# Kernel optimization log

Measured on AMD Instinct MI355X. Metric: run time of the kernel, lower is better.

The kernel has to match this reference:

```python
import jax, jax.numpy as jnp
import numpy as np

N = 50000      # nodes
E = 800000     # edges (before self loops)
IN = 128       # input_dim
H1, C1 = 4, 64   # conv1 heads, per-head channels (concat -> 256)
H2, C2 = 1, 64   # conv2 heads, per-head channels (concat=False -> 64)
EPS_BN = 1e-5
NEG_SLOPE = 0.2


def setup_inputs() -> dict:
    key = jax.random.key(0)
    ks = jax.random.split(key, 20)
    s = 0.05
    d = {}
    d["x"] = jax.random.normal(ks[0], (N, IN), dtype=jnp.float32)
    d["edge_index"] = jax.random.randint(ks[1], (2, E), 0, N, dtype=jnp.int32)
    # GATConv 1: lin weight [IN, H1*C1], att vectors [H1, C1], bias [H1*C1]
    d["W1"] = jax.random.normal(ks[2], (IN, H1 * C1), dtype=jnp.float32) * s
    d["a1_src"] = jax.random.normal(ks[3], (H1, C1), dtype=jnp.float32) * s
    d["a1_dst"] = jax.random.normal(ks[4], (H1, C1), dtype=jnp.float32) * s
    d["b1"] = jnp.zeros((H1 * C1,), jnp.float32)
    # GATConv 2 (concat=False): lin weight [H1*C1, H2*C2]
    d["W2"] = jax.random.normal(ks[5], (H1 * C1, H2 * C2), dtype=jnp.float32) * s
    d["a2_src"] = jax.random.normal(ks[6], (H2, C2), dtype=jnp.float32) * s
    d["a2_dst"] = jax.random.normal(ks[7], (H2, C2), dtype=jnp.float32) * s
    d["b2"] = jnp.zeros((C2,), jnp.float32)
    # projection Linear(output_dim -> input_dim)
    d["Wp"] = jax.random.normal(ks[8], (C2, IN), dtype=jnp.float32) * s
    d["bp"] = jnp.zeros((IN,), jnp.float32)
    # BatchNorm affine params
    d["g1"] = jnp.ones((H1 * C1,), jnp.float32); d["be1"] = jnp.zeros((H1 * C1,), jnp.float32)
    d["g2"] = jnp.ones((C2,), jnp.float32);      d["be2"] = jnp.zeros((C2,), jnp.float32)
    d["g3"] = jnp.ones((IN,), jnp.float32);      d["be3"] = jnp.zeros((IN,), jnp.float32)
    return d


def batch_norm(x, gamma, beta):
    mu = jnp.mean(x, axis=0, keepdims=True)
    var = jnp.var(x, axis=0, keepdims=True)
    return (x - mu) * jax.lax.rsqrt(var + EPS_BN) * gamma + beta


def gat_conv(x, src, dst, W, a_src, a_dst, bias, heads, out_ch, concat):
    n = x.shape[0]
    h = (x @ W).reshape(n, heads, out_ch)            # [N,H,C]
    alpha_s = jnp.einsum('nhc,hc->nh', h, a_src)     # [N,H]
    alpha_d = jnp.einsum('nhc,hc->nh', h, a_dst)
    e = jax.nn.leaky_relu(alpha_s[src] + alpha_d[dst], NEG_SLOPE)  # [E',H]
    # segment softmax over edges sharing the same destination node
    m = jax.ops.segment_max(e, dst, num_segments=n)
    m = jnp.where(jnp.isfinite(m), m, 0.0)
    ex = jnp.exp(e - m[dst])
    den = jax.ops.segment_sum(ex, dst, num_segments=n)
    alpha = ex / (den[dst] + 1e-16)                  # [E',H]
    msg = alpha[:, :, None] * h[src]                 # [E',H,C]
    out = jax.ops.segment_sum(msg, dst, num_segments=n)  # [N,H,C]
    if concat:
        out = out.reshape(n, heads * out_ch)
    else:
        out = out.mean(axis=1)
    return out + bias


def reference(x, edge_index, W1, a1_src, a1_dst, b1, W2, a2_src, a2_dst, b2,
              Wp, bp, g1, be1, g2, be2, g3, be3):
    n = x.shape[0]
    # PyG GATConv default add_self_loops=True
    loops = jnp.arange(n, dtype=edge_index.dtype)
    src = jnp.concatenate([edge_index[0], loops])
    dst = jnp.concatenate([edge_index[1], loops])
    h = gat_conv(x, src, dst, W1, a1_src, a1_dst, b1, H1, C1, True)
    h = jax.nn.elu(batch_norm(h, g1, be1))
    # dropout is a no-op in eval mode
    h = gat_conv(h, src, dst, W2, a2_src, a2_dst, b2, H2, C2, False)
    h = jax.nn.elu(batch_norm(h, g2, be2))
    h = h @ Wp + bp
    return batch_norm(h, g3, be3)
```

## Files before the change

kernel.cpp:

```cpp
#include <hip/hip_runtime.h>
#include <cstdint>
#include <cstddef>

#define NEG_SLOPE 0.2f
#define EPS_BN 1e-5f

typedef __bf16 bf16x8 __attribute__((ext_vector_type(8)));
typedef float  f32x4  __attribute__((ext_vector_type(4)));
typedef unsigned short ushort_t;

static __device__ __forceinline__ float lrelu(float x){ return x > 0.f ? x : NEG_SLOPE * x; }
static __device__ __forceinline__ float elu(float x){ return x > 0.f ? x : __expf(x) - 1.f; }

static __device__ __forceinline__ float bf2f(ushort_t u){
  union { unsigned i; float f; } c; c.i = ((unsigned)u) << 16; return c.f;
}
static __device__ __forceinline__ ushort_t f2bf(float f){
  unsigned u = __float_as_uint(f);
  u += 0x7fffu + ((u >> 16) & 1u);
  return (ushort_t)(u >> 16);
}
static __device__ __forceinline__ void unpk(unsigned u, float& lo, float& hi){
  lo = __uint_as_float(u << 16);
  hi = __uint_as_float(u & 0xffff0000u);
}

union BF8 { bf16x8 v; ushort_t u[8]; };

static inline int ceil_div(int a, int b){ return (a + b - 1) / b; }


__global__ void fill_u32_kernel(unsigned* __restrict__ p, unsigned v, int n){
  int i = blockIdx.x * 256 + threadIdx.x;
  if(i < n) p[i] = v;
}


__global__ void hist_kernel(const int* __restrict__ ei, int* __restrict__ deg, int E, int N){
  int e = blockIdx.x * 256 + threadIdx.x;
  if(e >= E + N) return;
  int d = (e < E) ? ei[E + e] : (e - E);
  atomicAdd(&deg[d], 1);
}

__global__ __launch_bounds__(256) void scan1_kernel(const int* __restrict__ deg, int* __restrict__ rowptr,
                                                    int* __restrict__ cur, int* __restrict__ partials,
                                                    unsigned* __restrict__ tick, int n){
  int t = threadIdx.x, lane = t & 63, wv = t >> 6;
  int base = blockIdx.x * 2048 + t * 8;
  int v[8]; int run = 0;
  #pragma unroll
  for(int k = 0; k < 8; k++){ int i = base + k; v[k] = (i < n) ? deg[i] : 0; run += v[k]; }
  int sc = run;
  #pragma unroll
  for(int off = 1; off < 64; off <<= 1){
    int u = __shfl_up(sc, off);
    if(lane >= off) sc += u;
  }
  __shared__ int wtot[4], woff[4];
  __shared__ bool slast;
  if(lane == 63) wtot[wv] = sc;
  __syncthreads();
  if(t == 0){
    int a = 0;
    #pragma unroll
    for(int i = 0; i < 4; i++){ woff[i] = a; a += wtot[i]; }
    partials[blockIdx.x] = a;
  }
  __syncthreads();
  int excl = (sc - run) + woff[wv];
  #pragma unroll
  for(int k = 0; k < 8; k++){
    int i = base + k;
    if(i < n){ cur[i] = excl; excl += v[k]; rowptr[i + 1] = excl; }
  }
  if(t == 0){
    __threadfence();
    slast = (atomicAdd(tick, 1u) == (unsigned)(gridDim.x - 1));
  }
  __syncthreads();
  if(slast && t < 64){
    int nb = gridDim.x;
    int pv = (t < nb) ? atomicAdd(&partials[t], 0) : 0;
    int psc = pv;
    #pragma unroll
    for(int off = 1; off < 64; off <<= 1){
      int u = __shfl_up(psc, off);
      if(t >= off) psc += u;
    }
    if(t < nb) partials[t] = psc - pv;
  }
}

__global__ void scan3_kernel(const int* __restrict__ partials, int* __restrict__ rowptr,
                             int* __restrict__ cur, int n){
  int i = blockIdx.x * 256 + threadIdx.x;
  if(i == 0) rowptr[0] = 0;
  if(i < n){
    int off = partials[i >> 11];
    rowptr[i + 1] += off;
    cur[i] += off;
  }
}

__global__ void scatter_kernel(const int* __restrict__ ei, int* __restrict__ cur,
                               int* __restrict__ col, int E, int N){
  int e = blockIdx.x * 256 + threadIdx.x;
  if(e >= E + N) return;
  int s, d;
  if(e < E){ s = ei[e]; d = ei[E + e]; } else { s = e - E; d = e - E; }
  int pos = atomicAdd(&cur[d], 1);
  col[pos] = s;
}


static __device__ void packW_body(const float* W, ushort_t* Wp, int K, int Nn, int idx){
  int lane = idx & 63;
  int rest = idx >> 6;
  int KS = K >> 5;
  int s = rest % KS, t = rest / KS;
  int n  = t * 16 + (lane & 15);
  int k0 = s * 32 + (lane >> 4) * 8;
  ushort_t tmp[8];
  #pragma unroll
  for(int j = 0; j < 8; j++) tmp[j] = f2bf(W[(size_t)(k0 + j) * Nn + n]);
  uint4 pk;
  pk.x = tmp[0] | ((unsigned)tmp[1] << 16);
  pk.y = tmp[2] | ((unsigned)tmp[3] << 16);
  pk.z = tmp[4] | ((unsigned)tmp[5] << 16);
  pk.w = tmp[6] | ((unsigned)tmp[7] << 16);
  *reinterpret_cast<uint4*>(Wp + (size_t)idx * 8) = pk;
}

__global__ void packW_all_kernel(const float* __restrict__ W1, const float* __restrict__ W2,
                                 const float* __restrict__ W3, ushort_t* __restrict__ W1p,
                                 ushort_t* __restrict__ W2p, ushort_t* __restrict__ W3p){
  int idx = blockIdx.x * 256 + threadIdx.x;
  if(idx < 4096)       packW_body(W1, W1p, 128, 256, idx);
  else if(idx < 6144)  packW_body(W2, W2p, 256, 64,  idx - 4096);
  else if(idx < 7168)  packW_body(W3, W3p, 64,  128, idx - 6144);
}


template<int K, int NT, int AMODE, int H>
__global__ __launch_bounds__(256) void gemm_kernel(const void* __restrict__ Asrc,
                                                   const ushort_t* __restrict__ Bp,
                                                   ushort_t* __restrict__ C, int M,
                                                   const float* __restrict__ scale,
                                                   const float* __restrict__ shift,
                                                   const float* __restrict__ a_src,
                                                   const float* __restrict__ a_dst,
                                                   float* __restrict__ as_,
                                                   float* __restrict__ ad_){
  constexpr int KS = K >> 5;
  int lane = threadIdx.x & 63, wv = threadIdx.x >> 6;
  int row0 = blockIdx.x * 64 + wv * 16;
  int mi = lane & 15, q = lane >> 4;
  int arow = row0 + mi; if(arow > M - 1) arow = M - 1;
  const bf16x8* bbase = reinterpret_cast<const bf16x8*>(Bp) + lane;
  f32x4 acc[NT] = {};
  #pragma unroll
  for(int s = 0; s < KS; s++){
    BF8 cv;
    if(AMODE == 0){
      const float* ap = (const float*)Asrc + (size_t)arow * K + s * 32 + q * 8;
      float4 u0 = *reinterpret_cast<const float4*>(ap);
      float4 u1 = *reinterpret_cast<const float4*>(ap + 4);
      cv.u[0] = f2bf(u0.x); cv.u[1] = f2bf(u0.y); cv.u[2] = f2bf(u0.z); cv.u[3] = f2bf(u0.w);
      cv.u[4] = f2bf(u1.x); cv.u[5] = f2bf(u1.y); cv.u[6] = f2bf(u1.z); cv.u[7] = f2bf(u1.w);
    } else {
      const ushort_t* ap = (const ushort_t*)Asrc + (size_t)arow * K + s * 32 + q * 8;
      uint4 u = *reinterpret_cast<const uint4*>(ap);
      int c0 = s * 32 + q * 8;
      float4 sc0 = *reinterpret_cast<const float4*>(scale + c0);
      float4 sc1 = *reinterpret_cast<const float4*>(scale + c0 + 4);
      float4 sh0 = *reinterpret_cast<const float4*>(shift + c0);
      float4 sh1 = *reinterpret_cast<const float4*>(shift + c0 + 4);
      float a, b;
      unpk(u.x, a, b); cv.u[0] = f2bf(elu(a * sc0.x + sh0.x)); cv.u[1] = f2bf(elu(b * sc0.y + sh0.y));
      unpk(u.y, a, b); cv.u[2] = f2bf(elu(a * sc0.z + sh0.z)); cv.u[3] = f2bf(elu(b * sc0.w + sh0.w));
      unpk(u.z, a, b); cv.u[4] = f2bf(elu(a * sc1.x + sh1.x)); cv.u[5] = f2bf(elu(b * sc1.y + sh1.y));
      unpk(u.w, a, b); cv.u[6] = f2bf(elu(a * sc1.z + sh1.z)); cv.u[7] = f2bf(elu(b * sc1.w + sh1.w));
    }
    bf16x8 af = cv.v;
    #pragma unroll
    for(int t = 0; t < NT; t++){
      bf16x8 bfr = bbase[((size_t)t * KS + s) * 64];
      acc[t] = __builtin_amdgcn_mfma_f32_16x16x32_bf16(af, bfr, acc[t], 0, 0, 0);
    }
  }
  #pragma unroll
  for(int t = 0; t < NT; t++){
    #pragma unroll
    for(int r = 0; r < 4; r++){
      int gr = row0 + q * 4 + r;
      if(gr < M) C[(size_t)gr * (NT * 16) + t * 16 + mi] = f2bf(acc[t][r]);
    }
  }
  if(H > 0){
    #pragma unroll
    for(int hh = 0; hh < H; hh++){
      #pragma unroll
      for(int r = 0; r < 4; r++){
        float ps = 0.f, pd = 0.f;
        #pragma unroll
        for(int tt = 0; tt < 4; tt++){
          int t = hh * 4 + tt;
          float av = acc[t][r];
          int c = t * 16 + mi;
          ps += av * a_src[c];
          pd += av * a_dst[c];
        }
        #pragma unroll
        for(int off = 1; off < 16; off <<= 1){
          ps += __shfl_xor(ps, off);
          pd += __shfl_xor(pd, off);
        }
        int gr = row0 + q * 4 + r;
        if(mi == 0 && gr < M){
          as_[(size_t)gr * H + hh] = ps;
          ad_[(size_t)gr * H + hh] = pd;
        }
      }
    }
  }
}


__global__ __launch_bounds__(256) void gat_agg4_kernel(const ushort_t* __restrict__ hfeat,
                                                       const float* __restrict__ as_,
                                                       const float* __restrict__ ad_,
                                                       const int* __restrict__ rowptr,
                                                       const int* __restrict__ col,
                                                       const float* __restrict__ bias,
                                                       ushort_t* __restrict__ out, int N){
  int wid = threadIdx.x >> 6, lane = threadIdx.x & 63;
  int n = blockIdx.x * 4 + wid;
  if(n > N - 1) n = N - 1;
  int start = rowptr[n], end = rowptr[n + 1];
  int g = lane >> 5, l = lane & 31, hidx = l >> 3;
  float adh = ad_[(size_t)n * 4 + hidx];
  float den = 0.f;
  float acc[8] = {};
  auto body = [&](int j){
    int s = col[j];
    float w = __expf(lrelu(as_[(size_t)s * 4 + hidx] + adh));
    uint4 u = *reinterpret_cast<const uint4*>(hfeat + (size_t)s * 256 + 8 * l);
    den += w;
    float a, b;
    unpk(u.x, a, b); acc[0] += w * a; acc[1] += w * b;
    unpk(u.y, a, b); acc[2] += w * a; acc[3] += w * b;
    unpk(u.z, a, b); acc[4] += w * a; acc[5] += w * b;
    unpk(u.w, a, b); acc[6] += w * a; acc[7] += w * b;
  };
  int j = start + g;
  for(; j + 6 < end; j += 8){ body(j); body(j + 2); body(j + 4); body(j + 6); }
  for(; j < end; j += 2) body(j);
  den += __shfl_xor(den, 32);
  #pragma unroll
  for(int k = 0; k < 8; k++) acc[k] += __shfl_xor(acc[k], 32);
  float dinv = 1.f / (den + 1e-16f);
  int cbase = 8 * l + g * 4;
  ushort_t o0 = f2bf(acc[g * 4 + 0] * dinv + bias[cbase + 0]);
  ushort_t o1 = f2bf(acc[g * 4 + 1] * dinv + bias[cbase + 1]);
  ushort_t o2 = f2bf(acc[g * 4 + 2] * dinv + bias[cbase + 2]);
  ushort_t o3 = f2bf(acc[g * 4 + 3] * dinv + bias[cbase + 3]);
  uint2 pk; pk.x = o0 | ((unsigned)o1 << 16); pk.y = o2 | ((unsigned)o3 << 16);
  *reinterpret_cast<uint2*>(out + (size_t)n * 256 + cbase) = pk;
}


__global__ __launch_bounds__(256) void gat_agg1_kernel(const ushort_t* __restrict__ hfeat,
                                                       const float* __restrict__ as_,
                                                       const float* __restrict__ ad_,
                                                       const int* __restrict__ rowptr,
                                                       const int* __restrict__ col,
                                                       const float* __restrict__ bias,
                                                       ushort_t* __restrict__ out, int N){
  int wid = threadIdx.x >> 6, lane = threadIdx.x & 63;
  int n = blockIdx.x * 4 + wid;
  if(n > N - 1) n = N - 1;
  int start = rowptr[n], end = rowptr[n + 1];
  int g = lane >> 4, l = lane & 15;
  float adn = ad_[n];
  float den = 0.f;
  float acc[4] = {};
  auto body = [&](int j){
    int s = col[j];
    float w = __expf(lrelu(as_[s] + adn));
    uint2 u = *reinterpret_cast<const uint2*>(hfeat + (size_t)s * 64 + 4 * l);
    den += w;
    float a, b;
    unpk(u.x, a, b); acc[0] += w * a; acc[1] += w * b;
    unpk(u.y, a, b); acc[2] += w * a; acc[3] += w * b;
  };
  int j = start + g;
  for(; j + 4 < end; j += 8){ body(j); body(j + 4); }
  if(j < end) body(j);
  den += __shfl_xor(den, 16); den += __shfl_xor(den, 32);
  #pragma unroll
  for(int k = 0; k < 4; k++){
    acc[k] += __shfl_xor(acc[k], 16);
    acc[k] += __shfl_xor(acc[k], 32);
  }
  float dinv = 1.f / (den + 1e-16f);
  if(g == 0){
    ushort_t o0 = f2bf(acc[0] * dinv + bias[4 * l + 0]);
    ushort_t o1 = f2bf(acc[1] * dinv + bias[4 * l + 1]);
    ushort_t o2 = f2bf(acc[2] * dinv + bias[4 * l + 2]);
    ushort_t o3 = f2bf(acc[3] * dinv + bias[4 * l + 3]);
    uint2 pk; pk.x = o0 | ((unsigned)o1 << 16); pk.y = o2 | ((unsigned)o3 << 16);
    *reinterpret_cast<uint2*>(out + (size_t)n * 64 + 4 * l) = pk;
  }
}


template<int C>
__global__ __launch_bounds__(256) void colstats_fin_kernel(const ushort_t* __restrict__ x, int N,
                                                           float* __restrict__ stats,
                                                           const float* __restrict__ gamma,
                                                           const float* __restrict__ beta,
                                                           float* __restrict__ scale,
                                                           float* __restrict__ shift,
                                                           unsigned* __restrict__ ticket, int nblk){
  constexpr int TPR = C / 8;
  constexpr int RPB = 256 / TPR;
  int t = threadIdx.x;
  int c0 = (t % TPR) * 8, rg = t / TPR;
  float sum[8] = {}, sq[8] = {};
  for(int r = blockIdx.x * RPB + rg; r < N; r += gridDim.x * RPB){
    uint4 u = *reinterpret_cast<const uint4*>(x + (size_t)r * C + c0);
    float a, b;
    unpk(u.x, a, b); sum[0] += a; sq[0] += a * a; sum[1] += b; sq[1] += b * b;
    unpk(u.y, a, b); sum[2] += a; sq[2] += a * a; sum[3] += b; sq[3] += b * b;
    unpk(u.z, a, b); sum[4] += a; sq[4] += a * a; sum[5] += b; sq[5] += b * b;
    unpk(u.w, a, b); sum[6] += a; sq[6] += a * a; sum[7] += b; sq[7] += b * b;
  }
  __shared__ float red[2][256][8];
  #pragma unroll
  for(int k = 0; k < 8; k++){ red[0][t][k] = sum[k]; red[1][t][k] = sq[k]; }
  __syncthreads();
  if(t < C){
    int tr = t >> 3, k = t & 7;
    float S = 0.f, Q = 0.f;
    for(int g2 = 0; g2 < RPB; g2++){
      S += red[0][g2 * TPR + tr][k];
      Q += red[1][g2 * TPR + tr][k];
    }
    atomicAdd(&stats[t], S);
    atomicAdd(&stats[C + t], Q);
  }
  __shared__ bool is_last;
  __syncthreads();
  if(t == 0){
    __threadfence();
    is_last = (atomicAdd(ticket, 1u) == (unsigned)(nblk - 1));
  }
  __syncthreads();
  if(is_last && t < C){
    float S = atomicAdd(&stats[t], 0.f);
    float Q = atomicAdd(&stats[C + t], 0.f);
    float invN = 1.f / (float)N;
    float mu = S * invN;
    float var = Q * invN - mu * mu;
    float rs = rsqrtf(var + EPS_BN);
    float scl = rs * gamma[t];
    scale[t] = scl;
    shift[t] = beta[t] - mu * scl;
  }
}


__global__ void bn3_kernel(const ushort_t* __restrict__ x, const float* __restrict__ scale,
                           const float* __restrict__ shift, float* __restrict__ y, long total4){
  long i = (long)blockIdx.x * 256 + threadIdx.x;
  if(i >= total4) return;
  long e0 = i * 4;
  int c0 = (int)(e0 & 127);
  uint2 u = *reinterpret_cast<const uint2*>(x + e0);
  float4 sc = *reinterpret_cast<const float4*>(scale + c0);
  float4 sh = *reinterpret_cast<const float4*>(shift + c0);
  float a, b;
  float4 o;
  unpk(u.x, a, b); o.x = a * sc.x + sh.x; o.y = b * sc.y + sh.y;
  unpk(u.y, a, b); o.z = a * sc.z + sh.z; o.w = b * sc.w + sh.w;
  *reinterpret_cast<float4*>(y + e0) = o;
}


extern "C" void kernel_launch(void* const* d_in, const int* in_sizes, int n_in,
                              void* d_out, int out_size, void* d_ws, size_t ws_size,
                              hipStream_t stream){
  const float* x   = (const float*)d_in[0];
  const int*   ei  = (const int*)  d_in[1];
  const float* W1  = (const float*)d_in[2];
  const float* a1s = (const float*)d_in[3];
  const float* a1d = (const float*)d_in[4];
  const float* b1  = (const float*)d_in[5];
  const float* W2  = (const float*)d_in[6];
  const float* a2s = (const float*)d_in[7];
  const float* a2d = (const float*)d_in[8];
  const float* b2  = (const float*)d_in[9];
  const float* Wp  = (const float*)d_in[10];
  const float* g1  = (const float*)d_in[12]; const float* be1 = (const float*)d_in[13];
  const float* g2  = (const float*)d_in[14]; const float* be2 = (const float*)d_in[15];
  const float* g3  = (const float*)d_in[16]; const float* be3 = (const float*)d_in[17];
  float* out = (float*)d_out;

  const int N  = in_sizes[0] / 128;
  const int E  = in_sizes[1] / 2;
  const int EP = E + N;
  const int Mpad = ((N + 63) / 64) * 64;
  const int NB = ceil_div(N, 2048);

  char* p = (char*)d_ws;
  auto carve = [&](size_t bytes) -> char* {
    char* r = p; p += (bytes + 255) & ~(size_t)255; return r;
  };
  float* meta   = (float*)carve(2048 * 4);
  int*   deg    = (int*)carve((size_t)N * 4);
  int*   cur    = (int*)carve((size_t)N * 4);
  int*   rowptr = (int*)carve((size_t)(N + 1) * 4);
  int*   col    = (int*)carve((size_t)EP * 4);
  int*   part   = (int*)carve(64 * 4);
  float* as_    = (float*)carve((size_t)N * 4 * 4);
  float* ad_    = (float*)carve((size_t)N * 4 * 4);
  ushort_t* W1p = (ushort_t*)carve((size_t)128 * 256 * 2);
  ushort_t* W2p = (ushort_t*)carve((size_t)256 * 64 * 2);
  ushort_t* W3p = (ushort_t*)carve((size_t)64 * 128 * 2);
  ushort_t* h1b   = (ushort_t*)carve((size_t)Mpad * 256 * 2);
  ushort_t* out1b = (ushort_t*)carve((size_t)Mpad * 256 * 2);
  ushort_t* h2b   = (ushort_t*)carve((size_t)Mpad * 64 * 2);
  ushort_t* out2b = (ushort_t*)carve((size_t)Mpad * 64 * 2);
  ushort_t* h3b   = (ushort_t*)carve((size_t)Mpad * 128 * 2);

  float* stats1 = meta;        float* scale1 = meta + 512;  float* shift1 = meta + 768;
  float* stats2 = meta + 1024; float* scale2 = meta + 1152; float* shift2 = meta + 1216;
  float* stats3 = meta + 1280; float* scale3 = meta + 1536; float* shift3 = meta + 1664;
  unsigned* tick = (unsigned*)(meta + 1792);

  fill_u32_kernel<<<ceil_div(N + 2048, 256), 256, 0, stream>>>((unsigned*)meta, 0u, N + 2048);
  hist_kernel<<<ceil_div(EP, 256), 256, 0, stream>>>(ei, deg, E, N);
  scan1_kernel<<<NB, 256, 0, stream>>>(deg, rowptr, cur, part, tick + 3, N);
  scan3_kernel<<<ceil_div(N, 256), 256, 0, stream>>>(part, rowptr, cur, N);
  scatter_kernel<<<ceil_div(EP, 256), 256, 0, stream>>>(ei, cur, col, E, N);
  packW_all_kernel<<<28, 256, 0, stream>>>(W1, W2, Wp, W1p, W2p, W3p);

  gemm_kernel<128, 16, 0, 4><<<Mpad / 64, 256, 0, stream>>>(x, W1p, h1b, N, nullptr, nullptr, a1s, a1d, as_, ad_);
  gat_agg4_kernel<<<ceil_div(N, 4), 256, 0, stream>>>(h1b, as_, ad_, rowptr, col, b1, out1b, N);
  colstats_fin_kernel<256><<<512, 256, 0, stream>>>(out1b, N, stats1, g1, be1, scale1, shift1, tick + 0, 512);

  gemm_kernel<256, 4, 1, 1><<<Mpad / 64, 256, 0, stream>>>(out1b, W2p, h2b, N, scale1, shift1, a2s, a2d, as_, ad_);
  gat_agg1_kernel<<<ceil_div(N, 4), 256, 0, stream>>>(h2b, as_, ad_, rowptr, col, b2, out2b, N);
  colstats_fin_kernel<64><<<512, 256, 0, stream>>>(out2b, N, stats2, g2, be2, scale2, shift2, tick + 1, 512);

  gemm_kernel<64, 8, 1, 0><<<Mpad / 64, 256, 0, stream>>>(out2b, W3p, h3b, N, scale2, shift2, nullptr, nullptr, nullptr, nullptr);
  colstats_fin_kernel<128><<<512, 256, 0, stream>>>(h3b, N, stats3, g3, be3, scale3, shift3, tick + 2, 512);
  bn3_kernel<<<ceil_div(N * 128 / 4, 256), 256, 0, stream>>>(h3b, scale3, shift3, out, (long)N * 32);
}
```

Measured before the change: 429.0 us.

## Fuse graph-build stages with weight packing and first GEMM, drop scan3 pass

Zero-fill is merged with weight packing, and the degree histogram runs in the same launch as the first GEMM, so the independent work overlaps and fewer kernels are launched. The scan3 fixup kernel and the cur array are removed. Scatter atomically increments the exclusive-scan rowptr and adds the block partial itself, and the aggregation kernels rebuild start and end from rowptr plus the partials. The aggregation loops are also made branchless with masked tail iterations. The cost is slightly more index arithmetic and some wasted loads on the padded tail lanes.

```diff
diff --git a/kernel.cpp b/kernel.cpp
--- a/kernel.cpp
+++ b/kernel.cpp
@@ -28,90 +28,6 @@
 union BF8 { bf16x8 v; ushort_t u[8]; };
 
 static inline int ceil_div(int a, int b){ return (a + b - 1) / b; }
-
-
-__global__ void fill_u32_kernel(unsigned* __restrict__ p, unsigned v, int n){
-  int i = blockIdx.x * 256 + threadIdx.x;
-  if(i < n) p[i] = v;
-}
-
-
-__global__ void hist_kernel(const int* __restrict__ ei, int* __restrict__ deg, int E, int N){
-  int e = blockIdx.x * 256 + threadIdx.x;
-  if(e >= E + N) return;
-  int d = (e < E) ? ei[E + e] : (e - E);
-  atomicAdd(&deg[d], 1);
-}
-
-__global__ __launch_bounds__(256) void scan1_kernel(const int* __restrict__ deg, int* __restrict__ rowptr,
-                                                    int* __restrict__ cur, int* __restrict__ partials,
-                                                    unsigned* __restrict__ tick, int n){
-  int t = threadIdx.x, lane = t & 63, wv = t >> 6;
-  int base = blockIdx.x * 2048 + t * 8;
-  int v[8]; int run = 0;
-  #pragma unroll
-  for(int k = 0; k < 8; k++){ int i = base + k; v[k] = (i < n) ? deg[i] : 0; run += v[k]; }
-  int sc = run;
-  #pragma unroll
-  for(int off = 1; off < 64; off <<= 1){
-    int u = __shfl_up(sc, off);
-    if(lane >= off) sc += u;
-  }
-  __shared__ int wtot[4], woff[4];
-  __shared__ bool slast;
-  if(lane == 63) wtot[wv] = sc;
-  __syncthreads();
-  if(t == 0){
-    int a = 0;
-    #pragma unroll
-    for(int i = 0; i < 4; i++){ woff[i] = a; a += wtot[i]; }
-    partials[blockIdx.x] = a;
-  }
-  __syncthreads();
-  int excl = (sc - run) + woff[wv];
-  #pragma unroll
-  for(int k = 0; k < 8; k++){
-    int i = base + k;
-    if(i < n){ cur[i] = excl; excl += v[k]; rowptr[i + 1] = excl; }
-  }
-  if(t == 0){
-    __threadfence();
-    slast = (atomicAdd(tick, 1u) == (unsigned)(gridDim.x - 1));
-  }
-  __syncthreads();
-  if(slast && t < 64){
-    int nb = gridDim.x;
-    int pv = (t < nb) ? atomicAdd(&partials[t], 0) : 0;
-    int psc = pv;
-    #pragma unroll
-    for(int off = 1; off < 64; off <<= 1){
-      int u = __shfl_up(psc, off);
-      if(t >= off) psc += u;
-    }
-    if(t < nb) partials[t] = psc - pv;
-  }
-}
-
-__global__ void scan3_kernel(const int* __restrict__ partials, int* __restrict__ rowptr,
-                             int* __restrict__ cur, int n){
-  int i = blockIdx.x * 256 + threadIdx.x;
-  if(i == 0) rowptr[0] = 0;
-  if(i < n){
-    int off = partials[i >> 11];
-    rowptr[i + 1] += off;
-    cur[i] += off;
-  }
-}
-
-__global__ void scatter_kernel(const int* __restrict__ ei, int* __restrict__ cur,
-                               int* __restrict__ col, int E, int N){
-  int e = blockIdx.x * 256 + threadIdx.x;
-  if(e >= E + N) return;
-  int s, d;
-  if(e < E){ s = ei[e]; d = ei[E + e]; } else { s = e - E; d = e - E; }
-  int pos = atomicAdd(&cur[d], 1);
-  col[pos] = s;
-}
 
 
 static __device__ void packW_body(const float* W, ushort_t* Wp, int K, int Nn, int idx){
@@ -132,29 +48,36 @@
   *reinterpret_cast<uint4*>(Wp + (size_t)idx * 8) = pk;
 }
 
-__global__ void packW_all_kernel(const float* __restrict__ W1, const float* __restrict__ W2,
-                                 const float* __restrict__ W3, ushort_t* __restrict__ W1p,
-                                 ushort_t* __restrict__ W2p, ushort_t* __restrict__ W3p){
-  int idx = blockIdx.x * 256 + threadIdx.x;
-  if(idx < 4096)       packW_body(W1, W1p, 128, 256, idx);
-  else if(idx < 6144)  packW_body(W2, W2p, 256, 64,  idx - 4096);
-  else if(idx < 7168)  packW_body(W3, W3p, 64,  128, idx - 6144);
+__global__ void init_kernel(unsigned* __restrict__ zbase, int ztotal,
+                            const float* __restrict__ W1, const float* __restrict__ W2,
+                            const float* __restrict__ W3, ushort_t* __restrict__ W1p,
+                            ushort_t* __restrict__ W2p, ushort_t* __restrict__ W3p){
+  int b = blockIdx.x;
+  if(b < 28){
+    int idx = b * 256 + threadIdx.x;
+    if(idx < 4096)       packW_body(W1, W1p, 128, 256, idx);
+    else if(idx < 6144)  packW_body(W2, W2p, 256, 64,  idx - 4096);
+    else if(idx < 7168)  packW_body(W3, W3p, 64,  128, idx - 6144);
+  } else {
+    int i = (b - 28) * 256 + threadIdx.x;
+    if(i < ztotal) zbase[i] = 0u;
+  }
 }
 
 
 template<int K, int NT, int AMODE, int H>
-__global__ __launch_bounds__(256) void gemm_kernel(const void* __restrict__ Asrc,
-                                                   const ushort_t* __restrict__ Bp,
-                                                   ushort_t* __restrict__ C, int M,
-                                                   const float* __restrict__ scale,
-                                                   const float* __restrict__ shift,
-                                                   const float* __restrict__ a_src,
-                                                   const float* __restrict__ a_dst,
-                                                   float* __restrict__ as_,
-                                                   float* __restrict__ ad_){
+static __device__ __forceinline__ void gemm_body(int bx, const void* __restrict__ Asrc,
+                                                 const ushort_t* __restrict__ Bp,
+                                                 ushort_t* __restrict__ C, int M,
+                                                 const float* __restrict__ scale,
+                                                 const float* __restrict__ shift,
+                                                 const float* __restrict__ a_src,
+                                                 const float* __restrict__ a_dst,
+                                                 float* __restrict__ as_,
+                                                 float* __restrict__ ad_){
   constexpr int KS = K >> 5;
   int lane = threadIdx.x & 63, wv = threadIdx.x >> 6;
-  int row0 = blockIdx.x * 64 + wv * 16;
+  int row0 = bx * 64 + wv * 16;
   int mi = lane & 15, q = lane >> 4;
   int arow = row0 + mi; if(arow > M - 1) arow = M - 1;
   const bf16x8* bbase = reinterpret_cast<const bf16x8*>(Bp) + lane;
@@ -226,25 +149,124 @@
   }
 }
 
+template<int K, int NT, int AMODE, int H>
+__global__ __launch_bounds__(256) void gemm_kernel(const void* __restrict__ Asrc,
+                                                   const ushort_t* __restrict__ Bp,
+                                                   ushort_t* __restrict__ C, int M,
+                                                   const float* __restrict__ scale,
+                                                   const float* __restrict__ shift,
+                                                   const float* __restrict__ a_src,
+                                                   const float* __restrict__ a_dst,
+                                                   float* __restrict__ as_,
+                                                   float* __restrict__ ad_){
+  gemm_body<K, NT, AMODE, H>(blockIdx.x, Asrc, Bp, C, M, scale, shift, a_src, a_dst, as_, ad_);
+}
+
+__global__ __launch_bounds__(256) void hist_gemm1_kernel(int GB, const int* __restrict__ ei,
+                                                         int* __restrict__ deg, int E, int N,
+                                                         const float* __restrict__ x,
+                                                         const ushort_t* __restrict__ W1p,
+                                                         ushort_t* __restrict__ h1b,
+                                                         const float* __restrict__ a1s,
+                                                         const float* __restrict__ a1d,
+                                                         float* __restrict__ as_,
+                                                         float* __restrict__ ad_){
+  int b = blockIdx.x;
+  if(b < GB){
+    gemm_body<128, 16, 0, 4>(b, x, W1p, h1b, N, nullptr, nullptr, a1s, a1d, as_, ad_);
+  } else {
+    int e = (b - GB) * 256 + threadIdx.x;
+    if(e < E + N){
+      int d = (e < E) ? ei[E + e] : (e - E);
+      atomicAdd(&deg[d], 1);
+    }
+  }
+}
+
+
+__global__ __launch_bounds__(256) void scan1_kernel(const int* __restrict__ deg, int* __restrict__ rowptr,
+                                                    int* __restrict__ partials,
+                                                    unsigned* __restrict__ tick, int n){
+  int t = threadIdx.x, lane = t & 63, wv = t >> 6;
+  int base = blockIdx.x * 2048 + t * 8;
+  int v[8]; int run = 0;
+  #pragma unroll
+  for(int k = 0; k < 8; k++){ int i = base + k; v[k] = (i < n) ? deg[i] : 0; run += v[k]; }
+  int sc = run;
+  #pragma unroll
+  for(int off = 1; off < 64; off <<= 1){
+    int u = __shfl_up(sc, off);
+    if(lane >= off) sc += u;
+  }
+  __shared__ int wtot[4], woff[4];
+  __shared__ bool slast;
+  if(lane == 63) wtot[wv] = sc;
+  __syncthreads();
+  if(t == 0){
+    int a = 0;
+    #pragma unroll
+    for(int i = 0; i < 4; i++){ woff[i] = a; a += wtot[i]; }
+    partials[blockIdx.x] = a;
+  }
+  __syncthreads();
+  int excl = (sc - run) + woff[wv];
+  #pragma unroll
+  for(int k = 0; k < 8; k++){
+    int i = base + k;
+    if(i < n){ rowptr[i] = excl; excl += v[k]; }
+  }
+  if(t == 0){
+    __threadfence();
+    slast = (atomicAdd(tick, 1u) == (unsigned)(gridDim.x - 1));
+  }
+  __syncthreads();
+  if(slast && t < 64){
+    int nb = gridDim.x;
+    int pv = (t < nb) ? atomicAdd(&partials[t], 0) : 0;
+    int psc = pv;
+    #pragma unroll
+    for(int off = 1; off < 64; off <<= 1){
+      int u = __shfl_up(psc, off);
+      if(t >= off) psc += u;
+    }
+    if(t < nb) partials[t] = psc - pv;
+  }
+}
+
+__global__ void scatter_kernel(const int* __restrict__ ei, int* __restrict__ rowptr,
+                               const int* __restrict__ part, int* __restrict__ col, int E, int N){
+  int e = blockIdx.x * 256 + threadIdx.x;
+  if(e >= E + N) return;
+  int s, d;
+  if(e < E){ s = ei[e]; d = ei[E + e]; } else { s = e - E; d = e - E; }
+  int pos = atomicAdd(&rowptr[d], 1) + part[d >> 11];
+  col[pos] = s;
+}
+
 
 __global__ __launch_bounds__(256) void gat_agg4_kernel(const ushort_t* __restrict__ hfeat,
                                                        const float* __restrict__ as_,
                                                        const float* __restrict__ ad_,
                                                        const int* __restrict__ rowptr,
+                                                       const int* __restrict__ part,
                                                        const int* __restrict__ col,
                                                        const float* __restrict__ bias,
                                                        ushort_t* __restrict__ out, int N){
   int wid = threadIdx.x >> 6, lane = threadIdx.x & 63;
   int n = blockIdx.x * 4 + wid;
   if(n > N - 1) n = N - 1;
-  int start = rowptr[n], end = rowptr[n + 1];
+  int start = n ? rowptr[n - 1] + part[(n - 1) >> 11] : 0;
+  int end   = rowptr[n] + part[n >> 11];
   int g = lane >> 5, l = lane & 31, hidx = l >> 3;
   float adh = ad_[(size_t)n * 4 + hidx];
   float den = 0.f;
   float acc[8] = {};
+  int last = end - 1;
   auto body = [&](int j){
-    int s = col[j];
-    float w = __expf(lrelu(as_[(size_t)s * 4 + hidx] + adh));
+    bool live = j < end;
+    int jc = live ? j : last;
+    int s = col[jc];
+    float w = live ? __expf(lrelu(as_[(size_t)s * 4 + hidx] + adh)) : 0.f;
     uint4 u = *reinterpret_cast<const uint4*>(hfeat + (size_t)s * 256 + 8 * l);
     den += w;
     float a, b;
@@ -253,9 +275,9 @@
     unpk(u.z, a, b); acc[4] += w * a; acc[5] += w * b;
     unpk(u.w, a, b); acc[6] += w * a; acc[7] += w * b;
   };
-  int j = start + g;
-  for(; j + 6 < end; j += 8){ body(j); body(j + 2); body(j + 4); body(j + 6); }
-  for(; j < end; j += 2) body(j);
+  for(int j = start + g; j < end; j += 8){
+    body(j); body(j + 2); body(j + 4); body(j + 6);
+  }
   den += __shfl_xor(den, 32);
   #pragma unroll
   for(int k = 0; k < 8; k++) acc[k] += __shfl_xor(acc[k], 32);
@@ -274,29 +296,34 @@
                                                        const float* __restrict__ as_,
                                                        const float* __restrict__ ad_,
                                                        const int* __restrict__ rowptr,
+                                                       const int* __restrict__ part,
                                                        const int* __restrict__ col,
                                                        const float* __restrict__ bias,
                                                        ushort_t* __restrict__ out, int N){
   int wid = threadIdx.x >> 6, lane = threadIdx.x & 63;
   int n = blockIdx.x * 4 + wid;
   if(n > N - 1) n = N - 1;
-  int start = rowptr[n], end = rowptr[n + 1];
+  int start = n ? rowptr[n - 1] + part[(n - 1) >> 11] : 0;
+  int end   = rowptr[n] + part[n >> 11];
   int g = lane >> 4, l = lane & 15;
   float adn = ad_[n];
   float den = 0.f;
   float acc[4] = {};
+  int last = end - 1;
   auto body = [&](int j){
-    int s = col[j];
-    float w = __expf(lrelu(as_[s] + adn));
+    bool live = j < end;
+    int jc = live ? j : last;
+    int s = col[jc];
+    float w = live ? __expf(lrelu(as_[s] + adn)) : 0.f;
     uint2 u = *reinterpret_cast<const uint2*>(hfeat + (size_t)s * 64 + 4 * l);
     den += w;
     float a, b;
     unpk(u.x, a, b); acc[0] += w * a; acc[1] += w * b;
     unpk(u.y, a, b); acc[2] += w * a; acc[3] += w * b;
   };
-  int j = start + g;
-  for(; j + 4 < end; j += 8){ body(j); body(j + 4); }
-  if(j < end) body(j);
+  for(int j = start + g; j < end; j += 16){
+    body(j); body(j + 4); body(j + 8); body(j + 12);
+  }
   den += __shfl_xor(den, 16); den += __shfl_xor(den, 32);
   #pragma unroll
   for(int k = 0; k < 4; k++){
@@ -412,6 +439,8 @@
   const int EP = E + N;
   const int Mpad = ((N + 63) / 64) * 64;
   const int NB = ceil_div(N, 2048);
+  const int GB = Mpad / 64;
+  const int HB = ceil_div(EP, 256);
 
   char* p = (char*)d_ws;
   auto carve = [&](size_t bytes) -> char* {
@@ -419,7 +448,6 @@
   };
   float* meta   = (float*)carve(2048 * 4);
   int*   deg    = (int*)carve((size_t)N * 4);
-  int*   cur    = (int*)carve((size_t)N * 4);
   int*   rowptr = (int*)carve((size_t)(N + 1) * 4);
   int*   col    = (int*)carve((size_t)EP * 4);
   int*   part   = (int*)carve(64 * 4);
@@ -439,22 +467,17 @@
   float* stats3 = meta + 1280; float* scale3 = meta + 1536; float* shift3 = meta + 1664;
   unsigned* tick = (unsigned*)(meta + 1792);
 
-  fill_u32_kernel<<<ceil_div(N + 2048, 256), 256, 0, stream>>>((unsigned*)meta, 0u, N + 2048);
-  hist_kernel<<<ceil_div(EP, 256), 256, 0, stream>>>(ei, deg, E, N);
-  scan1_kernel<<<NB, 256, 0, stream>>>(deg, rowptr, cur, part, tick + 3, N);
-  scan3_kernel<<<ceil_div(N, 256), 256, 0, stream>>>(part, rowptr, cur, N);
-  scatter_kernel<<<ceil_div(EP, 256), 256, 0, stream>>>(ei, cur, col, E, N);
-  packW_all_kernel<<<28, 256, 0, stream>>>(W1, W2, Wp, W1p, W2p, W3p);
-
-  gemm_kernel<128, 16, 0, 4><<<Mpad / 64, 256, 0, stream>>>(x, W1p, h1b, N, nullptr, nullptr, a1s, a1d, as_, ad_);
-  gat_agg4_kernel<<<ceil_div(N, 4), 256, 0, stream>>>(h1b, as_, ad_, rowptr, col, b1, out1b, N);
+  init_kernel<<<28 + ceil_div(N + 2048, 256), 256, 0, stream>>>((unsigned*)meta, N + 2048,
+                                                                W1, W2, Wp, W1p, W2p, W3p);
+  hist_gemm1_kernel<<<GB + HB, 256, 0, stream>>>(GB, ei, deg, E, N, x, W1p, h1b, a1s, a1d, as_, ad_);
+  scan1_kernel<<<NB, 256, 0, stream>>>(deg, rowptr, part, tick + 3, N);
+  scatter_kernel<<<HB, 256, 0, stream>>>(ei, rowptr, part, col, E, N);
+  gat_agg4_kernel<<<ceil_div(N, 4), 256, 0, stream>>>(h1b, as_, ad_, rowptr, part, col, b1, out1b, N);
   colstats_fin_kernel<256><<<512, 256, 0, stream>>>(out1b, N, stats1, g1, be1, scale1, shift1, tick + 0, 512);
-
-  gemm_kernel<256, 4, 1, 1><<<Mpad / 64, 256, 0, stream>>>(out1b, W2p, h2b, N, scale1, shift1, a2s, a2d, as_, ad_);
-  gat_agg1_kernel<<<ceil_div(N, 4), 256, 0, stream>>>(h2b, as_, ad_, rowptr, col, b2, out2b, N);
+  gemm_kernel<256, 4, 1, 1><<<GB, 256, 0, stream>>>(out1b, W2p, h2b, N, scale1, shift1, a2s, a2d, as_, ad_);
+  gat_agg1_kernel<<<ceil_div(N, 4), 256, 0, stream>>>(h2b, as_, ad_, rowptr, part, col, b2, out2b, N);
   colstats_fin_kernel<64><<<512, 256, 0, stream>>>(out2b, N, stats2, g2, be2, scale2, shift2, tick + 1, 512);
-
-  gemm_kernel<64, 8, 1, 0><<<Mpad / 64, 256, 0, stream>>>(out2b, W3p, h3b, N, scale2, shift2, nullptr, nullptr, nullptr, nullptr);
+  gemm_kernel<64, 8, 1, 0><<<GB, 256, 0, stream>>>(out2b, W3p, h3b, N, scale2, shift2, nullptr, nullptr, nullptr, nullptr);
   colstats_fin_kernel<128><<<512, 256, 0, stream>>>(h3b, N, stats3, g3, be3, scale3, shift3, tick + 2, 512);
   bn3_kernel<<<ceil_div(N * 128 / 4, 256), 256, 0, stream>>>(h3b, scale3, shift3, out, (long)N * 32);
 }
```

New measurement: 418.3 us. 1.03x faster.
